# Kernel optimization log

Measured on AMD Instinct MI355X. Metric: run time of the kernel, lower is better.

## Reference

```python
import jax, jax.numpy as jnp
import numpy as np

B, S, IN_DIM, D, H, L, C = 8, 1024, 256, 1024, 16, 6, 10
DK = D // H
EPS = 1e-5


def setup_inputs() -> dict:
    key = jax.random.key(0)
    ks = iter(jax.random.split(key, 64))
    n = lambda shape, s=0.02: jax.random.normal(next(ks), shape, dtype=jnp.float32) * s
    inp = {
        'x': jax.random.normal(next(ks), (B, S, IN_DIM), dtype=jnp.float32),
        'emb_w': n((IN_DIM, D)), 'emb_b': jnp.zeros((D,), jnp.float32),
        'Wq': n((L, D, D)), 'bq': jnp.zeros((L, D), jnp.float32),
        'Wk': n((L, D, D)), 'bk': jnp.zeros((L, D), jnp.float32),
        'Wv': n((L, D, D)), 'bv': jnp.zeros((L, D), jnp.float32),
        'Wo': n((L, D, D)), 'bo': jnp.zeros((L, D), jnp.float32),
        'W1': n((L, D, 4 * D)), 'b1': jnp.zeros((L, 4 * D), jnp.float32),
        'W2': n((L, 4 * D, D)), 'b2': jnp.zeros((L, D), jnp.float32),
        'ln1_s': jnp.ones((L, D), jnp.float32), 'ln1_b': jnp.zeros((L, D), jnp.float32),
        'ln2_s': jnp.ones((L, D), jnp.float32), 'ln2_b': jnp.zeros((L, D), jnp.float32),
        'fc_w': n((D, C)), 'fc_b': jnp.zeros((C,), jnp.float32),
    }
    return inp


def _pos_encoding_rows(n_rows):
    # Faithful to the torch module: pe is [max_len,1,D]; pe[:x.size(0)] picks the
    # first `batch` positions and broadcasts over the sequence dim.
    pos = jnp.arange(n_rows, dtype=jnp.float32)[:, None]
    div = jnp.exp(jnp.arange(0, D, 2, dtype=jnp.float32) * (-np.log(10000.0) / D))
    pe = jnp.zeros((n_rows, D), jnp.float32)
    pe = pe.at[:, 0::2].set(jnp.sin(pos * div)).at[:, 1::2].set(jnp.cos(pos * div))
    return pe


def _layer_norm(x, scale, bias):
    mu = jnp.mean(x, axis=-1, keepdims=True)
    var = jnp.mean(jnp.square(x - mu), axis=-1, keepdims=True)
    return (x - mu) * jax.lax.rsqrt(var + EPS) * scale + bias


def reference(x, emb_w, emb_b, Wq, bq, Wk, bk, Wv, bv, Wo, bo,
              W1, b1, W2, b2, ln1_s, ln1_b, ln2_s, ln2_b, fc_w, fc_b):
    h = x @ emb_w + emb_b                              # [B,S,D]
    h = h + _pos_encoding_rows(B)[:, None, :]          # broadcast pe[:B] over seq
    scale = 1.0 / np.sqrt(DK)
    for i in range(L):
        def heads(y, W, b):
            return (y @ W + b).reshape(B, S, H, DK).transpose(0, 2, 1, 3)  # bhsd
        q = heads(h, Wq[i], bq[i])
        k = heads(h, Wk[i], bk[i])
        v = heads(h, Wv[i], bv[i])
        scores = jnp.einsum('bhqd,bhkd->bhqk', q, k) * scale
        p = jax.nn.softmax(scores, axis=-1)
        o = jnp.einsum('bhqk,bhkd->bhqd', p, v)
        o = o.transpose(0, 2, 1, 3).reshape(B, S, D)
        attn_out = o @ Wo[i] + bo[i]
        h = _layer_norm(h + attn_out, ln1_s[i], ln1_b[i])
        ff = jax.nn.relu(h @ W1[i] + b1[i]) @ W2[i] + b2[i]
        h = _layer_norm(h + ff, ln2_s[i], ln2_b[i])
    pooled = jnp.mean(h, axis=1)                       # [B,D]
    return pooled @ fc_w + fc_b                        # [B,C]
```

## Files before the change

### kernel.cpp

```cpp
#include <hip/hip_runtime.h>
#include <stdint.h>

#define B_   8
#define S_   1024
#define IND  256
#define D_   1024
#define H_   16
#define DKH  64
#define L_   6
#define FF   4096
#define NTOK (B_*S_)

typedef __bf16 bf16;
typedef __attribute__((ext_vector_type(4))) float  f32x4;
typedef __attribute__((ext_vector_type(8))) __bf16 bf16x8;
typedef __attribute__((ext_vector_type(4))) __bf16 bf16x4;
typedef __attribute__((ext_vector_type(2))) __bf16 bf16x2;

#define AS1 __attribute__((address_space(1)))
#define AS3 __attribute__((address_space(3)))

__device__ __forceinline__ void gload16(const void* g, void* l) {
  __builtin_amdgcn_global_load_lds((AS1 void*)(const_cast<void*>(g)), (AS3 void*)l, 16, 0, 0);
}

__global__ __launch_bounds__(256)
void k_trans(const float* __restrict__ in, bf16* __restrict__ out,
             int K, int N, long inStride, long outStride) {
  __shared__ float t[32][33];
  const float* inp = in + (long)blockIdx.z * inStride;
  bf16* outp = out + (long)blockIdx.z * outStride;
  const int n0 = blockIdx.x * 32, k0 = blockIdx.y * 32;
  const int tx = threadIdx.x & 31, ty = threadIdx.x >> 5;
  #pragma unroll
  for (int j = 0; j < 32; j += 8)
    t[ty + j][tx] = inp[(long)(k0 + ty + j) * N + n0 + tx];
  __syncthreads();
  #pragma unroll
  for (int j = 0; j < 32; j += 8)
    outp[(long)(n0 + ty + j) * K + k0 + tx] = (bf16)t[tx][ty + j];
}

__global__ __launch_bounds__(256)
void k_f2b(const float* __restrict__ in, bf16* __restrict__ out) {
  const long i = ((long)blockIdx.x * 256 + threadIdx.x) * 4;
  f32x4 v = *(const f32x4*)(in + i);
  bf16x4 o;
  #pragma unroll
  for (int j = 0; j < 4; ++j) o[j] = (bf16)v[j];
  *(bf16x4*)(out + i) = o;
}

__global__ __launch_bounds__(256)
void k_pe(float* __restrict__ pe) {
  const int i = blockIdx.x * 256 + threadIdx.x;
  const int b = i >> 10, d = i & 1023;
  const float k2 = (float)(d & ~1);
  const float dv = __expf(k2 * (-9.210340371976184f / (float)D_));
  const float a = (float)b * dv;
  pe[i] = (d & 1) ? cosf(a) : sinf(a);
}

__global__ __launch_bounds__(256)
void k_packb(const float* __restrict__ bq, const float* __restrict__ bk,
             const float* __restrict__ bv, float* __restrict__ out) {
  const int i = blockIdx.x * 256 + threadIdx.x;
  const int l = i / 3072, j = i % 3072;
  const float* src = (j < 1024) ? bq : ((j < 2048) ? bk : bv);
  out[i] = src[l * 1024 + (j & 1023)];
}

template<int EPI>
__global__ __launch_bounds__(256)
void k_gemm(const bf16* __restrict__ A, const bf16* __restrict__ Bt,
            const float* __restrict__ bias,
            void* __restrict__ out0, void* __restrict__ out1,
            const float* __restrict__ pe,
            int M, int N, int K) {
  __shared__ __align__(16) bf16 sA[128 * 32];
  __shared__ __align__(16) bf16 sB[128 * 32];
  const int tid = threadIdx.x;
  const int lane = tid & 63, wv = tid >> 6;
  const int bx = blockIdx.x, by = blockIdx.y;
  const int wm = wv >> 1, wn = wv & 1;
  const int lg = lane >> 4, lc = lane & 15;
  const long arow0 = (long)by * 128;
  const long brow0 = (long)bx * 128;
  const int c0 = (wv * 2 + 0) * 64 + lane;
  const int c1 = (wv * 2 + 1) * 64 + lane;
  const int r0 = c0 >> 2, s0 = c0 & 3;
  const int r1 = c1 >> 2, s1 = c1 & 3;
  bf16* ldsA0 = sA + (wv * 2 + 0) * 512;
  bf16* ldsA1 = sA + (wv * 2 + 1) * 512;
  bf16* ldsB0 = sB + (wv * 2 + 0) * 512;
  bf16* ldsB1 = sB + (wv * 2 + 1) * 512;
  const bf16* Ab = A + arow0 * K;
  const bf16* Bb = Bt + brow0 * K;
  f32x4 acc[4][4] = {};
  const int kT = K >> 5;
  for (int kt = 0; kt < kT; ++kt) {
    const int k0 = kt << 5;
    gload16(Ab + (long)r0 * K + k0 + s0 * 8, ldsA0);
    gload16(Ab + (long)r1 * K + k0 + s1 * 8, ldsA1);
    gload16(Bb + (long)r0 * K + k0 + s0 * 8, ldsB0);
    gload16(Bb + (long)r1 * K + k0 + s1 * 8, ldsB1);
    __syncthreads();
    bf16x8 af[4], bfr[4];
    #pragma unroll
    for (int mr = 0; mr < 4; ++mr)
      af[mr] = *(const bf16x8*)(sA + (wm * 64 + mr * 16 + lc) * 32 + lg * 8);
    #pragma unroll
    for (int nc = 0; nc < 4; ++nc)
      bfr[nc] = *(const bf16x8*)(sB + (wn * 64 + nc * 16 + lc) * 32 + lg * 8);
    #pragma unroll
    for (int mr = 0; mr < 4; ++mr)
      #pragma unroll
      for (int nc = 0; nc < 4; ++nc)
        acc[mr][nc] = __builtin_amdgcn_mfma_f32_16x16x32_bf16(af[mr], bfr[nc], acc[mr][nc], 0, 0, 0);
    __syncthreads();
  }
  #pragma unroll
  for (int mr = 0; mr < 4; ++mr) {
    const int row0 = by * 128 + wm * 64 + mr * 16 + lg * 4;
    #pragma unroll
    for (int nc = 0; nc < 4; ++nc) {
      const int col = bx * 128 + wn * 64 + nc * 16 + lc;
      const float bvv = bias[col];
      #pragma unroll
      for (int r = 0; r < 4; ++r) {
        float v = acc[mr][nc][r] + bvv;
        const long rr = row0 + r;
        if constexpr (EPI == 0) {
          ((bf16*)out0)[rr * N + col] = (bf16)v;
        } else {
          const long bb = rr >> 10;
          v += pe[bb * D_ + col];
          ((float*)out0)[rr * N + col] = v;
          ((bf16*)out1)[rr * N + col] = (bf16)v;
        }
      }
    }
  }
}

template<int EPI, int SPLIT>
__global__ __launch_bounds__(512, 2)
void k_gemm256(const bf16* __restrict__ A, const bf16* __restrict__ Bt,
               const float* __restrict__ bias,
               void* __restrict__ out0, void* __restrict__ out1,
               float* __restrict__ pout0, float* __restrict__ pout1,
               int M, int N, int K) {
  __shared__ __align__(16) bf16 lds[65536];
  const int tid = threadIdx.x;
  const int lane = tid & 63, wv = tid >> 6;
  const int wm = wv >> 2, wn = wv & 3;
  const int lg = lane >> 4, lc = lane & 15;
  const int gx = gridDim.x;
  const int nwg = gx * gridDim.y;
  int bid = blockIdx.x + blockIdx.y * gx;
  const int cpx = nwg >> 3;
  bid = (bid & 7) * cpx + (bid >> 3);
  const int bxs = bid % gx, bys = bid / gx;
  const int tileRow = bys * 256, tileCol = bxs * 256;
  const int kHalf = SPLIT ? (K >> 1) : K;
  const long kOff = SPLIT ? (long)blockIdx.z * kHalf : 0;
  const bf16* Abase = A + (long)tileRow * K + kOff;
  const bf16* Bbase = Bt + (long)tileCol * K + kOff;
  const long laneOff = (long)lc * K + lg * 8;
  f32x4 acc[8][4] = {};
  const int NT = kHalf >> 6;
  const int NI = NT >> 1;

  auto stA = [&](int t, int h, int bb) {
    const int rg = h * 16 + wv * 2;
    const int mb = rg >> 1;
    const bf16* s = Abase + (long)(mb * 16) * K + t * 64 + laneOff;
    bf16* d = lds + bb * 32768 + rg * 512;
    gload16(s, d);
    gload16(s + 32, d + 512);
  };
  auto stB = [&](int t, int h, int bb) {
    const int rg = h * 16 + wv * 2;
    const int mb = rg >> 1;
    const bf16* s = Bbase + (long)(mb * 16) * K + t * 64 + laneOff;
    bf16* d = lds + bb * 32768 + 16384 + rg * 512;
    gload16(s, d);
    gload16(s + 32, d + 512);
  };

  bf16x8 aF[8];
  bf16x8 bF0[4], bF1[4];

#define LDA(BB, MH) do { _Pragma("unroll") for (int m = 0; m < 4; ++m) \
    _Pragma("unroll") for (int kk = 0; kk < 2; ++kk) \
      aF[m*2+kk] = *(const bf16x8*)(lds + (BB)*32768 + ((wm*8 + (MH)*4 + m)*2 + kk)*512 + lane*8); \
  } while(0)
#define LDB(BB, NH, DST) do { _Pragma("unroll") for (int n = 0; n < 2; ++n) \
    _Pragma("unroll") for (int kk = 0; kk < 2; ++kk) \
      DST[n*2+kk] = *(const bf16x8*)(lds + (BB)*32768 + 16384 + ((wn*4 + (NH)*2 + n)*2 + kk)*512 + lane*8); \
  } while(0)
#define MMA(MH, NH, BSRC) do { \
    __builtin_amdgcn_s_setprio(1); \
    _Pragma("unroll") for (int m = 0; m < 4; ++m) \
      _Pragma("unroll") for (int n = 0; n < 2; ++n) { \
        acc[(MH)*4+m][(NH)*2+n] = __builtin_amdgcn_mfma_f32_16x16x32_bf16(aF[m*2+0], BSRC[n*2+0], acc[(MH)*4+m][(NH)*2+n], 0, 0, 0); \
        acc[(MH)*4+m][(NH)*2+n] = __builtin_amdgcn_mfma_f32_16x16x32_bf16(aF[m*2+1], BSRC[n*2+1], acc[(MH)*4+m][(NH)*2+n], 0, 0, 0); \
      } \
    __builtin_amdgcn_s_setprio(0); \
  } while(0)
#define VM8 asm volatile("s_waitcnt vmcnt(8)" ::: "memory")
#define VM0 asm volatile("s_waitcnt vmcnt(0)" ::: "memory")
#define BAR __builtin_amdgcn_s_barrier()

  stA(0, 0, 0); stB(0, 0, 0); stA(0, 1, 0); stB(0, 1, 0);
  stA(1, 0, 1); stB(1, 0, 1); stA(1, 1, 1); stB(1, 1, 1);

  for (int i = 0; i < NI - 1; ++i) {
    const int t2 = 2 * i + 2, t3 = 2 * i + 3;
    VM8; BAR; LDA(0, 0); LDB(0, 0, bF0);                    MMA(0, 0, bF0);
         BAR; LDB(0, 1, bF1); stA(t2, 0, 0);                MMA(0, 1, bF1);
         BAR; LDA(0, 1);      stB(t2, 0, 0);                MMA(1, 0, bF0);
         BAR;                 stA(t2, 1, 0); stB(t2, 1, 0); MMA(1, 1, bF1);
    VM8; BAR; LDA(1, 0); LDB(1, 0, bF0);                    MMA(0, 0, bF0);
         BAR; LDB(1, 1, bF1); stA(t3, 0, 1);                MMA(0, 1, bF1);
         BAR; LDA(1, 1);      stB(t3, 0, 1);                MMA(1, 0, bF0);
         BAR;                 stA(t3, 1, 1); stB(t3, 1, 1); MMA(1, 1, bF1);
  }
  {
    VM8; BAR; LDA(0, 0); LDB(0, 0, bF0); MMA(0, 0, bF0);
         BAR; LDB(0, 1, bF1);            MMA(0, 1, bF1);
         BAR; LDA(0, 1);                 MMA(1, 0, bF0);
         BAR;                            MMA(1, 1, bF1);
    VM0; BAR; LDA(1, 0); LDB(1, 0, bF0); MMA(0, 0, bF0);
         BAR; LDB(1, 1, bF1);            MMA(0, 1, bF1);
         BAR; LDA(1, 1);                 MMA(1, 0, bF0);
         BAR;                            MMA(1, 1, bF1);
  }
#undef LDA
#undef LDB
#undef MMA
#undef VM8
#undef VM0
#undef BAR

  #pragma unroll
  for (int mr = 0; mr < 8; ++mr) {
    const int row0 = tileRow + wm * 128 + mr * 16 + lg * 4;
    #pragma unroll
    for (int nr = 0; nr < 4; ++nr) {
      const int col = tileCol + wn * 64 + nr * 16 + lc;
      if constexpr (SPLIT) {
        float* po = blockIdx.z ? pout1 : pout0;
        #pragma unroll
        for (int r = 0; r < 4; ++r)
          po[(long)(row0 + r) * N + col] = acc[mr][nr][r];
      } else if constexpr (EPI == 2) {
        const float bvv = bias[col];
        const int which = col >> 10;
        const int hh = (col & 1023) >> 6;
        const int dk = col & 63;
        const long bb = row0 >> 10;
        const int sr = row0 & 1023;
        if (which == 2) {
          bf16x4 pk;
          #pragma unroll
          for (int r = 0; r < 4; ++r) pk[r] = (bf16)(acc[mr][nr][r] + bvv);
          *(bf16x4*)((bf16*)out1 + ((bb * H_ + hh) * (long)DKH + dk) * S_ + sr) = pk;
        } else {
          #pragma unroll
          for (int r = 0; r < 4; ++r) {
            float v = acc[mr][nr][r] + bvv;
            if (which == 0) v *= 0.125f;
            ((bf16*)out0)[(long)which * NTOK * D_ + ((bb * H_ + hh) * (long)S_ + sr + r) * DKH + dk] = (bf16)v;
          }
        }
      } else {
        const float bvv = bias[col];
        #pragma unroll
        for (int r = 0; r < 4; ++r) {
          float v = acc[mr][nr][r] + bvv;
          const long rr = row0 + r;
          if constexpr (EPI == 1) v = fmaxf(v, 0.f);
          ((bf16*)out0)[rr * N + col] = (bf16)v;
        }
      }
    }
  }
}

__global__ __launch_bounds__(256)
void k_flash(const bf16* __restrict__ qg, const bf16* __restrict__ kgl,
             const bf16* __restrict__ vtg, bf16* __restrict__ og) {
  __shared__ __align__(16) bf16 sK[64 * 64];
  __shared__ __align__(16) bf16 sV[64 * 64];
  __shared__ __align__(16) bf16 sP[4 * 16 * 64];
  const int tid = threadIdx.x, lane = tid & 63, wv = tid >> 6;
  const int lg = lane >> 4, lc = lane & 15;
  int bid = blockIdx.x + blockIdx.y * 16;
  bid = (bid & 7) * 256 + (bid >> 3);
  const int qt = bid & 15, bh = bid >> 4;
  const long base = (long)bh * S_ * DKH;
  const bf16* qb = qg + base;
  const bf16* kb = kgl + base;
  const bf16* vb = vtg + base;
  const int qrow = qt * 64 + wv * 16 + lc;
  const bf16x8 qf0 = *(const bf16x8*)(qb + (long)qrow * DKH + lg * 8);
  const bf16x8 qf1 = *(const bf16x8*)(qb + (long)qrow * DKH + 32 + lg * 8);
  float mrun = -3e38f, lrun = 0.f;
  f32x4 oacc[4] = {};
  bf16* sPw = sP + wv * (16 * 64);
  const int swzP = (lc & 7) << 4;
  const int c0 = wv * 128 + lane, c1 = c0 + 64;
  const int r0 = c0 >> 3, sl0 = (c0 & 7) ^ (r0 & 7);
  const int r1 = c1 >> 3, sl1 = (c1 & 7) ^ (r1 & 7);
  bf16* dst0 = sK + c0 * 8 - lane * 8;
  bf16* dst1 = sK + c1 * 8 - lane * 8;
  bf16* dstV0 = sV + c0 * 8 - lane * 8;
  bf16* dstV1 = sV + c1 * 8 - lane * 8;
  for (int kt = 0; kt < S_ / 64; ++kt) {
    const int gk = kt * 64;
    gload16(kb + (long)(gk + r0) * DKH + sl0 * 8, dst0);
    gload16(kb + (long)(gk + r1) * DKH + sl1 * 8, dst1);
    gload16(vb + (long)r0 * S_ + gk + sl0 * 8, dstV0);
    gload16(vb + (long)r1 * S_ + gk + sl1 * 8, dstV1);
    __syncthreads();
    f32x4 sacc[4] = {};
    #pragma unroll
    for (int nc = 0; nc < 4; ++nc) {
      const int kr = nc * 16 + lc;
      bf16x8 k0 = *(const bf16x8*)((char*)sK + kr * 128 + (((0 + lg) ^ (kr & 7)) << 4));
      bf16x8 k1 = *(const bf16x8*)((char*)sK + kr * 128 + (((4 + lg) ^ (kr & 7)) << 4));
      sacc[nc] = __builtin_amdgcn_mfma_f32_16x16x32_bf16(k0, qf0, sacc[nc], 0, 0, 0);
      sacc[nc] = __builtin_amdgcn_mfma_f32_16x16x32_bf16(k1, qf1, sacc[nc], 0, 0, 0);
    }
    float pm = sacc[0][0];
    #pragma unroll
    for (int nc = 0; nc < 4; ++nc)
      #pragma unroll
      for (int r = 0; r < 4; ++r) pm = fmaxf(pm, sacc[nc][r]);
    pm = fmaxf(pm, __shfl_xor(pm, 16));
    pm = fmaxf(pm, __shfl_xor(pm, 32));
    const float mnew = fmaxf(mrun, pm);
    const float fac = __expf(mrun - mnew);
    float ps = 0.f;
    #pragma unroll
    for (int nc = 0; nc < 4; ++nc)
      #pragma unroll
      for (int r = 0; r < 4; ++r) {
        const float p = __expf(sacc[nc][r] - mnew);
        sacc[nc][r] = p;
        ps += p;
      }
    ps += __shfl_xor(ps, 16);
    ps += __shfl_xor(ps, 32);
    lrun = lrun * fac + ps;
    mrun = mnew;
    #pragma unroll
    for (int nc = 0; nc < 4; ++nc)
      #pragma unroll
      for (int rp = 0; rp < 2; ++rp) {
        bf16x2 t;
        t[0] = (bf16)sacc[nc][rp * 2 + 0];
        t[1] = (bf16)sacc[nc][rp * 2 + 1];
        *(bf16x2*)((char*)sPw + lc * 128 + ((nc * 32 + lg * 8 + rp * 4) ^ swzP)) = t;
      }
    asm volatile("s_waitcnt lgkmcnt(0)" ::: "memory");
    __builtin_amdgcn_sched_barrier(0);
    float fr[4];
    #pragma unroll
    for (int r = 0; r < 4; ++r) fr[r] = __shfl(fac, lg * 4 + r);
    #pragma unroll
    for (int nc = 0; nc < 4; ++nc)
      #pragma unroll
      for (int r = 0; r < 4; ++r) oacc[nc][r] *= fr[r];
    #pragma unroll
    for (int m = 0; m < 2; ++m) {
      const bf16x8 pf = *(const bf16x8*)((char*)sPw + lc * 128 + ((m * 64 + lg * 16) ^ swzP));
      #pragma unroll
      for (int nc = 0; nc < 4; ++nc) {
        const int vr = nc * 16 + lc;
        bf16x8 vf = *(const bf16x8*)((char*)sV + vr * 128 + (((m * 4 + lg) ^ (vr & 7)) << 4));
        oacc[nc] = __builtin_amdgcn_mfma_f32_16x16x32_bf16(pf, vf, oacc[nc], 0, 0, 0);
      }
    }
    __syncthreads();
  }
  const int b = bh >> 4, h = bh & 15;
  const float linv = 1.f / lrun;
  #pragma unroll
  for (int r = 0; r < 4; ++r) {
    const float inv = __shfl(linv, lg * 4 + r);
    const int s = qt * 64 + wv * 16 + lg * 4 + r;
    const long obase = (((long)b * S_ + s) * H_ + h) * DKH;
    #pragma unroll
    for (int nc = 0; nc < 4; ++nc)
      og[obase + nc * 16 + lc] = (bf16)(oacc[nc][r] * inv);
  }
}

template<int TWO>
__global__ __launch_bounds__(256)
void k_addln(const float* __restrict__ hin, const bf16* __restrict__ dlt,
             const float* __restrict__ p0, const float* __restrict__ p1,
             const float* __restrict__ gb,
             const float* __restrict__ sc, const float* __restrict__ bi,
             float* __restrict__ hout, bf16* __restrict__ hbout) {
  const int row = blockIdx.x, t = threadIdx.x;
  const long off = (long)row * D_ + t * 4;
  f32x4 hv = *(const f32x4*)(hin + off);
  f32x4 x;
  if constexpr (TWO) {
    f32x4 a = *(const f32x4*)(p0 + off);
    f32x4 b = *(const f32x4*)(p1 + off);
    f32x4 g = *(const f32x4*)(gb + t * 4);
    #pragma unroll
    for (int j = 0; j < 4; ++j) x[j] = hv[j] + a[j] + b[j] + g[j];
  } else {
    bf16x4 dv = *(const bf16x4*)(dlt + off);
    #pragma unroll
    for (int j = 0; j < 4; ++j) x[j] = hv[j] + (float)dv[j];
  }
  float s = 0.f, ss = 0.f;
  #pragma unroll
  for (int j = 0; j < 4; ++j) { s += x[j]; ss += x[j] * x[j]; }
  #pragma unroll
  for (int m = 1; m < 64; m <<= 1) { s += __shfl_xor(s, m); ss += __shfl_xor(ss, m); }
  __shared__ float red[8];
  const int w = t >> 6, ln = t & 63;
  if (ln == 0) { red[w] = s; red[4 + w] = ss; }
  __syncthreads();
  s = red[0] + red[1] + red[2] + red[3];
  ss = red[4] + red[5] + red[6] + red[7];
  const float mu = s * (1.f / D_);
  const float rstd = rsqrtf(ss * (1.f / D_) - mu * mu + 1e-5f);
  f32x4 scv = *(const f32x4*)(sc + t * 4);
  f32x4 biv = *(const f32x4*)(bi + t * 4);
  f32x4 y; bf16x4 yb;
  #pragma unroll
  for (int j = 0; j < 4; ++j) { y[j] = (x[j] - mu) * rstd * scv[j] + biv[j]; yb[j] = (bf16)y[j]; }
  *(f32x4*)(hout + off) = y;
  *(bf16x4*)(hbout + off) = yb;
}

__global__ __launch_bounds__(256)
void k_pool1(const float* __restrict__ h, float* __restrict__ part) {
  const int i = blockIdx.x * 256 + threadIdx.x;
  const int b = i >> 10, d = i & 1023;
  const int s0 = blockIdx.y * 128;
  float s = 0.f;
  for (int t = 0; t < 128; ++t) s += h[((long)b * S_ + s0 + t) * D_ + d];
  part[(long)blockIdx.y * NTOK + i] = s;
}

__global__ __launch_bounds__(256)
void k_pool2(const float* __restrict__ part, float* __restrict__ pooled) {
  const int i = blockIdx.x * 256 + threadIdx.x;
  float s = 0.f;
  #pragma unroll
  for (int j = 0; j < 8; ++j) s += part[(long)j * NTOK + i];
  pooled[i] = s * (1.f / S_);
}

__global__ __launch_bounds__(64)
void k_fc(const float* __restrict__ pooled, const float* __restrict__ fw,
          const float* __restrict__ fb, float* __restrict__ out) {
  const int b = blockIdx.x / 10, c = blockIdx.x % 10;
  const int lane = threadIdx.x;
  float s = 0.f;
  for (int d = lane; d < D_; d += 64) s += pooled[b * D_ + d] * fw[d * 10 + c];
  #pragma unroll
  for (int m = 1; m < 64; m <<= 1) s += __shfl_xor(s, m);
  if (lane == 0) out[b * 10 + c] = s + fb[c];
}

extern "C" void kernel_launch(void* const* d_in, const int* in_sizes, int n_in,
                              void* d_out, int out_size, void* d_ws, size_t ws_size,
                              hipStream_t stream) {
  const float* x     = (const float*)d_in[0];
  const float* emb_w = (const float*)d_in[1];
  const float* emb_b = (const float*)d_in[2];
  const float* Wq    = (const float*)d_in[3];
  const float* bq    = (const float*)d_in[4];
  const float* Wk    = (const float*)d_in[5];
  const float* bk    = (const float*)d_in[6];
  const float* Wv    = (const float*)d_in[7];
  const float* bv    = (const float*)d_in[8];
  const float* Wo    = (const float*)d_in[9];
  const float* bo    = (const float*)d_in[10];
  const float* W1    = (const float*)d_in[11];
  const float* b1    = (const float*)d_in[12];
  const float* W2    = (const float*)d_in[13];
  const float* b2    = (const float*)d_in[14];
  const float* ln1s  = (const float*)d_in[15];
  const float* ln1b  = (const float*)d_in[16];
  const float* ln2s  = (const float*)d_in[17];
  const float* ln2b  = (const float*)d_in[18];
  const float* fcw   = (const float*)d_in[19];
  const float* fcb   = (const float*)d_in[20];

  char* w = (char*)d_ws;
  size_t off = 0;
  auto alloc = [&](size_t bytes) -> char* {
    char* p = w + off;
    off += (bytes + 255) & ~(size_t)255;
    return p;
  };
  bf16*  x_bf  = (bf16*) alloc((size_t)NTOK * IND * 2);
  bf16*  embT  = (bf16*) alloc((size_t)D_ * IND * 2);
  bf16*  qkvT  = (bf16*) alloc((size_t)L_ * 3 * D_ * D_ * 2);
  bf16*  woT   = (bf16*) alloc((size_t)L_ * D_ * D_ * 2);
  bf16*  w1T   = (bf16*) alloc((size_t)L_ * FF * D_ * 2);
  bf16*  w2T   = (bf16*) alloc((size_t)L_ * D_ * FF * 2);
  float* qkvB  = (float*)alloc((size_t)L_ * 3 * D_ * 4);
  float* pe    = (float*)alloc((size_t)B_ * D_ * 4);
  float* h_f   = (float*)alloc((size_t)NTOK * D_ * 4);
  bf16*  h_b   = (bf16*) alloc((size_t)NTOK * D_ * 2);
  bf16*  delta = (bf16*) alloc((size_t)NTOK * D_ * 2);
  float* pooled= (float*)alloc((size_t)B_ * D_ * 4);
  float* part  = (float*)alloc((size_t)8 * NTOK * 4);
  bf16*  scratch = (bf16*)alloc((size_t)NTOK * FF * 2);
  bf16* qb  = scratch;
  bf16* kb  = scratch + (size_t)NTOK * D_;
  bf16* vTb = scratch + (size_t)2 * NTOK * D_;
  bf16* ob  = scratch + (size_t)3 * NTOK * D_;
  bf16* ffn1 = scratch;
  float* p0 = (float*)alloc((size_t)NTOK * D_ * 4);
  float* p1 = (float*)alloc((size_t)NTOK * D_ * 4);
  const bool canSplit = (off <= ws_size);
  (void)in_sizes; (void)n_in; (void)out_size;

  k_f2b<<<dim3(NTOK * IND / 1024), dim3(256), 0, stream>>>(x, x_bf);
  k_trans<<<dim3(D_ / 32, IND / 32, 1), dim3(256), 0, stream>>>(emb_w, embT, IND, D_, 0, 0);
  k_trans<<<dim3(32, 32, L_), dim3(256), 0, stream>>>(Wq, qkvT,               D_, D_, (long)D_ * D_, (long)3 * D_ * D_);
  k_trans<<<dim3(32, 32, L_), dim3(256), 0, stream>>>(Wk, qkvT + D_ * D_,     D_, D_, (long)D_ * D_, (long)3 * D_ * D_);
  k_trans<<<dim3(32, 32, L_), dim3(256), 0, stream>>>(Wv, qkvT + 2 * D_ * D_, D_, D_, (long)D_ * D_, (long)3 * D_ * D_);
  k_trans<<<dim3(32, 32, L_), dim3(256), 0, stream>>>(Wo, woT, D_, D_, (long)D_ * D_, (long)D_ * D_);
  k_trans<<<dim3(FF / 32, 32, L_), dim3(256), 0, stream>>>(W1, w1T, D_, FF, (long)D_ * FF, (long)FF * D_);
  k_trans<<<dim3(32, FF / 32, L_), dim3(256), 0, stream>>>(W2, w2T, FF, D_, (long)FF * D_, (long)D_ * FF);
  k_pe<<<dim3(B_ * D_ / 256), dim3(256), 0, stream>>>(pe);
  k_packb<<<dim3(L_ * 3 * D_ / 256), dim3(256), 0, stream>>>(bq, bk, bv, qkvB);

  k_gemm<3><<<dim3(D_ / 128, NTOK / 128), dim3(256), 0, stream>>>(
      x_bf, embT, emb_b, h_f, h_b, pe, NTOK, D_, IND);

  for (int l = 0; l < L_; ++l) {
    k_gemm256<2, 0><<<dim3(3 * D_ / 256, NTOK / 256), dim3(512), 0, stream>>>(
        h_b, qkvT + (size_t)l * 3 * D_ * D_, qkvB + l * 3 * D_,
        qb, vTb, nullptr, nullptr, NTOK, 3 * D_, D_);
    k_flash<<<dim3(S_ / 64, B_ * H_), dim3(256), 0, stream>>>(qb, kb, vTb, ob);
    if (canSplit) {
      k_gemm256<0, 1><<<dim3(D_ / 256, NTOK / 256, 2), dim3(512), 0, stream>>>(
          ob, woT + (size_t)l * D_ * D_, nullptr,
          nullptr, nullptr, p0, p1, NTOK, D_, D_);
      k_addln<1><<<dim3(NTOK), dim3(256), 0, stream>>>(
          h_f, nullptr, p0, p1, bo + l * D_, ln1s + l * D_, ln1b + l * D_, h_f, h_b);
    } else {
      k_gemm256<0, 0><<<dim3(D_ / 256, NTOK / 256), dim3(512), 0, stream>>>(
          ob, woT + (size_t)l * D_ * D_, bo + l * D_,
          delta, nullptr, nullptr, nullptr, NTOK, D_, D_);
      k_addln<0><<<dim3(NTOK), dim3(256), 0, stream>>>(
          h_f, delta, nullptr, nullptr, nullptr, ln1s + l * D_, ln1b + l * D_, h_f, h_b);
    }
    k_gemm256<1, 0><<<dim3(FF / 256, NTOK / 256), dim3(512), 0, stream>>>(
        h_b, w1T + (size_t)l * FF * D_, b1 + l * FF,
        ffn1, nullptr, nullptr, nullptr, NTOK, FF, D_);
    if (canSplit) {
      k_gemm256<0, 1><<<dim3(D_ / 256, NTOK / 256, 2), dim3(512), 0, stream>>>(
          ffn1, w2T + (size_t)l * D_ * FF, nullptr,
          nullptr, nullptr, p0, p1, NTOK, D_, FF);
      k_addln<1><<<dim3(NTOK), dim3(256), 0, stream>>>(
          h_f, nullptr, p0, p1, b2 + l * D_, ln2s + l * D_, ln2b + l * D_, h_f, h_b);
    } else {
      k_gemm256<0, 0><<<dim3(D_ / 256, NTOK / 256), dim3(512), 0, stream>>>(
          ffn1, w2T + (size_t)l * D_ * FF, b2 + l * D_,
          delta, nullptr, nullptr, nullptr, NTOK, D_, FF);
      k_addln<0><<<dim3(NTOK), dim3(256), 0, stream>>>(
          h_f, delta, nullptr, nullptr, nullptr, ln2s + l * D_, ln2b + l * D_, h_f, h_b);
    }
  }

  k_pool1<<<dim3(NTOK / 256, 8), dim3(256), 0, stream>>>(h_f, part);
  k_pool2<<<dim3(NTOK / 256), dim3(256), 0, stream>>>(part, pooled);
  k_fc<<<dim3(B_ * 10), dim3(64), 0, stream>>>(pooled, fcw, fcb, (float*)d_out);
}
```

Measured before the change: 2.358 ms.

## Restructure 256x256 GEMM mainloop into 4-slot K=32 ring-buffer pipeline

```diff
diff --git a/kernel.cpp b/kernel.cpp
--- a/kernel.cpp
+++ b/kernel.cpp
@@ -162,86 +162,61 @@
   bid = (bid & 7) * cpx + (bid >> 3);
   const int bxs = bid % gx, bys = bid / gx;
   const int tileRow = bys * 256, tileCol = bxs * 256;
-  const int kHalf = SPLIT ? (K >> 1) : K;
-  const long kOff = SPLIT ? (long)blockIdx.z * kHalf : 0;
+  const int kPart = SPLIT ? (K >> 1) : K;
+  const long kOff = SPLIT ? (long)blockIdx.z * kPart : 0;
   const bf16* Abase = A + (long)tileRow * K + kOff;
   const bf16* Bbase = Bt + (long)tileCol * K + kOff;
   const long laneOff = (long)lc * K + lg * 8;
   f32x4 acc[8][4] = {};
-  const int NT = kHalf >> 6;
-  const int NI = NT >> 1;
-
-  auto stA = [&](int t, int h, int bb) {
-    const int rg = h * 16 + wv * 2;
-    const int mb = rg >> 1;
-    const bf16* s = Abase + (long)(mb * 16) * K + t * 64 + laneOff;
-    bf16* d = lds + bb * 32768 + rg * 512;
-    gload16(s, d);
-    gload16(s + 32, d + 512);
+  const int NT = kPart >> 5;
+
+  const int rgA = wv * 2;
+  auto stage = [&](int t) {
+    const int slot = (t & 3) * 16384;
+    const bf16* sa = Abase + (long)(rgA * 16) * K + t * 32 + laneOff;
+    const bf16* sb = Bbase + (long)(rgA * 16) * K + t * 32 + laneOff;
+    gload16(sa,                lds + slot + rgA * 512);
+    gload16(sa + (long)16 * K, lds + slot + rgA * 512 + 512);
+    gload16(sb,                lds + slot + 8192 + rgA * 512);
+    gload16(sb + (long)16 * K, lds + slot + 8192 + rgA * 512 + 512);
   };
-  auto stB = [&](int t, int h, int bb) {
-    const int rg = h * 16 + wv * 2;
-    const int mb = rg >> 1;
-    const bf16* s = Bbase + (long)(mb * 16) * K + t * 64 + laneOff;
-    bf16* d = lds + bb * 32768 + 16384 + rg * 512;
-    gload16(s, d);
-    gload16(s + 32, d + 512);
+
+  auto compute = [&](int t, bool doStage, int ts) {
+    const int slot = (t & 3) * 16384;
+    __builtin_amdgcn_s_barrier();
+    __builtin_amdgcn_sched_barrier(0);
+    if (doStage) stage(ts);
+    bf16x8 aF[8], bF[4];
+    #pragma unroll
+    for (int m = 0; m < 8; ++m)
+      aF[m] = *(const bf16x8*)(lds + slot + (wm * 8 + m) * 512 + lane * 8);
+    #pragma unroll
+    for (int n = 0; n < 4; ++n)
+      bF[n] = *(const bf16x8*)(lds + slot + 8192 + (wn * 4 + n) * 512 + lane * 8);
+    __builtin_amdgcn_sched_barrier(0);
+    __builtin_amdgcn_s_setprio(1);
+    #pragma unroll
+    for (int m = 0; m < 8; ++m)
+      #pragma unroll
+      for (int n = 0; n < 4; ++n)
+        acc[m][n] = __builtin_amdgcn_mfma_f32_16x16x32_bf16(aF[m], bF[n], acc[m][n], 0, 0, 0);
+    __builtin_amdgcn_s_setprio(0);
   };
 
-  bf16x8 aF[8];
-  bf16x8 bF0[4], bF1[4];
-
-#define LDA(BB, MH) do { _Pragma("unroll") for (int m = 0; m < 4; ++m) \
-    _Pragma("unroll") for (int kk = 0; kk < 2; ++kk) \
-      aF[m*2+kk] = *(const bf16x8*)(lds + (BB)*32768 + ((wm*8 + (MH)*4 + m)*2 + kk)*512 + lane*8); \
-  } while(0)
-#define LDB(BB, NH, DST) do { _Pragma("unroll") for (int n = 0; n < 2; ++n) \
-    _Pragma("unroll") for (int kk = 0; kk < 2; ++kk) \
-      DST[n*2+kk] = *(const bf16x8*)(lds + (BB)*32768 + 16384 + ((wn*4 + (NH)*2 + n)*2 + kk)*512 + lane*8); \
-  } while(0)
-#define MMA(MH, NH, BSRC) do { \
-    __builtin_amdgcn_s_setprio(1); \
-    _Pragma("unroll") for (int m = 0; m < 4; ++m) \
-      _Pragma("unroll") for (int n = 0; n < 2; ++n) { \
-        acc[(MH)*4+m][(NH)*2+n] = __builtin_amdgcn_mfma_f32_16x16x32_bf16(aF[m*2+0], BSRC[n*2+0], acc[(MH)*4+m][(NH)*2+n], 0, 0, 0); \
-        acc[(MH)*4+m][(NH)*2+n] = __builtin_amdgcn_mfma_f32_16x16x32_bf16(aF[m*2+1], BSRC[n*2+1], acc[(MH)*4+m][(NH)*2+n], 0, 0, 0); \
-      } \
-    __builtin_amdgcn_s_setprio(0); \
-  } while(0)
 #define VM8 asm volatile("s_waitcnt vmcnt(8)" ::: "memory")
+#define VM4 asm volatile("s_waitcnt vmcnt(4)" ::: "memory")
 #define VM0 asm volatile("s_waitcnt vmcnt(0)" ::: "memory")
-#define BAR __builtin_amdgcn_s_barrier()
-
-  stA(0, 0, 0); stB(0, 0, 0); stA(0, 1, 0); stB(0, 1, 0);
-  stA(1, 0, 1); stB(1, 0, 1); stA(1, 1, 1); stB(1, 1, 1);
-
-  for (int i = 0; i < NI - 1; ++i) {
-    const int t2 = 2 * i + 2, t3 = 2 * i + 3;
-    VM8; BAR; LDA(0, 0); LDB(0, 0, bF0);                    MMA(0, 0, bF0);
-         BAR; LDB(0, 1, bF1); stA(t2, 0, 0);                MMA(0, 1, bF1);
-         BAR; LDA(0, 1);      stB(t2, 0, 0);                MMA(1, 0, bF0);
-         BAR;                 stA(t2, 1, 0); stB(t2, 1, 0); MMA(1, 1, bF1);
-    VM8; BAR; LDA(1, 0); LDB(1, 0, bF0);                    MMA(0, 0, bF0);
-         BAR; LDB(1, 1, bF1); stA(t3, 0, 1);                MMA(0, 1, bF1);
-         BAR; LDA(1, 1);      stB(t3, 0, 1);                MMA(1, 0, bF0);
-         BAR;                 stA(t3, 1, 1); stB(t3, 1, 1); MMA(1, 1, bF1);
-  }
-  {
-    VM8; BAR; LDA(0, 0); LDB(0, 0, bF0); MMA(0, 0, bF0);
-         BAR; LDB(0, 1, bF1);            MMA(0, 1, bF1);
-         BAR; LDA(0, 1);                 MMA(1, 0, bF0);
-         BAR;                            MMA(1, 1, bF1);
-    VM0; BAR; LDA(1, 0); LDB(1, 0, bF0); MMA(0, 0, bF0);
-         BAR; LDB(1, 1, bF1);            MMA(0, 1, bF1);
-         BAR; LDA(1, 1);                 MMA(1, 0, bF0);
-         BAR;                            MMA(1, 1, bF1);
-  }
-#undef LDA
-#undef LDB
-#undef MMA
+
+  stage(0); stage(1); stage(2);
+  int t = 0;
+  for (; t < NT - 3; ++t) { VM8; compute(t, true, t + 3); }
+  VM8; compute(NT - 3, false, 0);
+  VM4; compute(NT - 2, false, 0);
+  VM0; compute(NT - 1, false, 0);
+
 #undef VM8
+#undef VM4
 #undef VM0
-#undef BAR
 
   #pragma unroll
   for (int mr = 0; mr < 8; ++mr) {
```

After: 2.392 ms. Within noise of the previous version (+1.5%).

## Restructure GEMM main loop into explicit barrier-bracketed phases with full-tile staging

Applied to the files above, without the earlier changes.

```diff
diff --git a/kernel.cpp b/kernel.cpp
--- a/kernel.cpp
+++ b/kernel.cpp
@@ -162,30 +162,27 @@
   bid = (bid & 7) * cpx + (bid >> 3);
   const int bxs = bid % gx, bys = bid / gx;
   const int tileRow = bys * 256, tileCol = bxs * 256;
-  const int kHalf = SPLIT ? (K >> 1) : K;
-  const long kOff = SPLIT ? (long)blockIdx.z * kHalf : 0;
+  const int kPart = SPLIT ? (K >> 1) : K;
+  const long kOff = SPLIT ? (long)blockIdx.z * kPart : 0;
   const bf16* Abase = A + (long)tileRow * K + kOff;
   const bf16* Bbase = Bt + (long)tileCol * K + kOff;
   const long laneOff = (long)lc * K + lg * 8;
   f32x4 acc[8][4] = {};
-  const int NT = kHalf >> 6;
+  const int NT = kPart >> 6;
   const int NI = NT >> 1;
 
-  auto stA = [&](int t, int h, int bb) {
-    const int rg = h * 16 + wv * 2;
-    const int mb = rg >> 1;
-    const bf16* s = Abase + (long)(mb * 16) * K + t * 64 + laneOff;
-    bf16* d = lds + bb * 32768 + rg * 512;
-    gload16(s, d);
-    gload16(s + 32, d + 512);
-  };
-  auto stB = [&](int t, int h, int bb) {
-    const int rg = h * 16 + wv * 2;
-    const int mb = rg >> 1;
-    const bf16* s = Bbase + (long)(mb * 16) * K + t * 64 + laneOff;
-    bf16* d = lds + bb * 32768 + 16384 + rg * 512;
-    gload16(s, d);
-    gload16(s + 32, d + 512);
+  auto stageFull = [&](int t, int bb) {
+    #pragma unroll
+    for (int h = 0; h < 2; ++h) {
+      const int rg = h * 16 + wv * 2;
+      const int mb = rg >> 1;
+      const bf16* sa = Abase + (long)(mb * 16) * K + t * 64 + laneOff;
+      const bf16* sb = Bbase + (long)(mb * 16) * K + t * 64 + laneOff;
+      bf16* da = lds + bb * 32768 + rg * 512;
+      bf16* db = lds + bb * 32768 + 16384 + rg * 512;
+      gload16(sa, da);      gload16(sa + 32, da + 512);
+      gload16(sb, db);      gload16(sb + 32, db + 512);
+    }
   };
 
   bf16x8 aF[8];
@@ -200,48 +197,69 @@
       DST[n*2+kk] = *(const bf16x8*)(lds + (BB)*32768 + 16384 + ((wn*4 + (NH)*2 + n)*2 + kk)*512 + lane*8); \
   } while(0)
 #define MMA(MH, NH, BSRC) do { \
-    __builtin_amdgcn_s_setprio(1); \
     _Pragma("unroll") for (int m = 0; m < 4; ++m) \
       _Pragma("unroll") for (int n = 0; n < 2; ++n) { \
         acc[(MH)*4+m][(NH)*2+n] = __builtin_amdgcn_mfma_f32_16x16x32_bf16(aF[m*2+0], BSRC[n*2+0], acc[(MH)*4+m][(NH)*2+n], 0, 0, 0); \
         acc[(MH)*4+m][(NH)*2+n] = __builtin_amdgcn_mfma_f32_16x16x32_bf16(aF[m*2+1], BSRC[n*2+1], acc[(MH)*4+m][(NH)*2+n], 0, 0, 0); \
       } \
+  } while(0)
+#define PH_R(RD, MH, NH, BSRC) do { \
+    RD; \
+    __builtin_amdgcn_sched_barrier(0); \
+    __builtin_amdgcn_s_barrier(); \
+    asm volatile("s_waitcnt lgkmcnt(0)" ::: "memory"); \
+    __builtin_amdgcn_sched_barrier(0); \
+    __builtin_amdgcn_s_setprio(1); \
+    MMA(MH, NH, BSRC); \
     __builtin_amdgcn_s_setprio(0); \
+    __builtin_amdgcn_s_barrier(); \
   } while(0)
-#define VM8 asm volatile("s_waitcnt vmcnt(8)" ::: "memory")
-#define VM0 asm volatile("s_waitcnt vmcnt(0)" ::: "memory")
-#define BAR __builtin_amdgcn_s_barrier()
-
-  stA(0, 0, 0); stB(0, 0, 0); stA(0, 1, 0); stB(0, 1, 0);
-  stA(1, 0, 1); stB(1, 0, 1); stA(1, 1, 1); stB(1, 1, 1);
+#define PH_S(STG, VMW, MH, NH, BSRC) do { \
+    STG; \
+    asm volatile("s_waitcnt " VMW ::: "memory"); \
+    __builtin_amdgcn_sched_barrier(0); \
+    __builtin_amdgcn_s_barrier(); \
+    __builtin_amdgcn_s_setprio(1); \
+    MMA(MH, NH, BSRC); \
+    __builtin_amdgcn_s_setprio(0); \
+    __builtin_amdgcn_s_barrier(); \
+  } while(0)
+
+  stageFull(0, 0);
+  stageFull(1, 1);
+  asm volatile("s_waitcnt vmcnt(8)" ::: "memory");
+  __builtin_amdgcn_s_barrier();
 
   for (int i = 0; i < NI - 1; ++i) {
     const int t2 = 2 * i + 2, t3 = 2 * i + 3;
-    VM8; BAR; LDA(0, 0); LDB(0, 0, bF0);                    MMA(0, 0, bF0);
-         BAR; LDB(0, 1, bF1); stA(t2, 0, 0);                MMA(0, 1, bF1);
-         BAR; LDA(0, 1);      stB(t2, 0, 0);                MMA(1, 0, bF0);
-         BAR;                 stA(t2, 1, 0); stB(t2, 1, 0); MMA(1, 1, bF1);
-    VM8; BAR; LDA(1, 0); LDB(1, 0, bF0);                    MMA(0, 0, bF0);
-         BAR; LDB(1, 1, bF1); stA(t3, 0, 1);                MMA(0, 1, bF1);
-         BAR; LDA(1, 1);      stB(t3, 0, 1);                MMA(1, 0, bF0);
-         BAR;                 stA(t3, 1, 1); stB(t3, 1, 1); MMA(1, 1, bF1);
+    PH_R(LDA(0, 0); LDB(0, 0, bF0), 0, 0, bF0);
+    PH_R(LDB(0, 1, bF1),            0, 1, bF1);
+    PH_R(LDA(0, 1),                 1, 0, bF0);
+    PH_S(stageFull(t2, 0), "vmcnt(8)", 1, 1, bF1);
+    PH_R(LDA(1, 0); LDB(1, 0, bF0), 0, 0, bF0);
+    PH_R(LDB(1, 1, bF1),            0, 1, bF1);
+    PH_R(LDA(1, 1),                 1, 0, bF0);
+    PH_S(stageFull(t3, 1), "vmcnt(8)", 1, 1, bF1);
   }
   {
-    VM8; BAR; LDA(0, 0); LDB(0, 0, bF0); MMA(0, 0, bF0);
-         BAR; LDB(0, 1, bF1);            MMA(0, 1, bF1);
-         BAR; LDA(0, 1);                 MMA(1, 0, bF0);
-         BAR;                            MMA(1, 1, bF1);
-    VM0; BAR; LDA(1, 0); LDB(1, 0, bF0); MMA(0, 0, bF0);
-         BAR; LDB(1, 1, bF1);            MMA(0, 1, bF1);
-         BAR; LDA(1, 1);                 MMA(1, 0, bF0);
-         BAR;                            MMA(1, 1, bF1);
+    PH_R(LDA(0, 0); LDB(0, 0, bF0), 0, 0, bF0);
+    PH_R(LDB(0, 1, bF1),            0, 1, bF1);
+    PH_R(LDA(0, 1),                 1, 0, bF0);
+    PH_S(, "vmcnt(0)", 1, 1, bF1);
+    PH_R(LDA(1, 0); LDB(1, 0, bF0), 0, 0, bF0);
+    PH_R(LDB(1, 1, bF1),            0, 1, bF1);
+    PH_R(LDA(1, 1),                 1, 0, bF0);
+    {
+      __builtin_amdgcn_s_setprio(1);
+      MMA(1, 1, bF1);
+      __builtin_amdgcn_s_setprio(0);
+    }
   }
 #undef LDA
 #undef LDB
 #undef MMA
-#undef VM8
-#undef VM0
-#undef BAR
+#undef PH_R
+#undef PH_S
 
   #pragma unroll
   for (int mr = 0; mr < 8; ++mr) {
```

Measured after the change: 2.612 ms. 10.8% more time.

## Double-buffer flash attention K/V tiles and batch GEMM stage loads

Applied to the files above, without the earlier changes.

```diff
diff --git a/kernel.cpp b/kernel.cpp
--- a/kernel.cpp
+++ b/kernel.cpp
@@ -162,30 +162,27 @@
   bid = (bid & 7) * cpx + (bid >> 3);
   const int bxs = bid % gx, bys = bid / gx;
   const int tileRow = bys * 256, tileCol = bxs * 256;
-  const int kHalf = SPLIT ? (K >> 1) : K;
-  const long kOff = SPLIT ? (long)blockIdx.z * kHalf : 0;
+  const int kPart = SPLIT ? (K >> 1) : K;
+  const long kOff = SPLIT ? (long)blockIdx.z * kPart : 0;
   const bf16* Abase = A + (long)tileRow * K + kOff;
   const bf16* Bbase = Bt + (long)tileCol * K + kOff;
   const long laneOff = (long)lc * K + lg * 8;
   f32x4 acc[8][4] = {};
-  const int NT = kHalf >> 6;
+  const int NT = kPart >> 6;
   const int NI = NT >> 1;
 
-  auto stA = [&](int t, int h, int bb) {
-    const int rg = h * 16 + wv * 2;
-    const int mb = rg >> 1;
-    const bf16* s = Abase + (long)(mb * 16) * K + t * 64 + laneOff;
-    bf16* d = lds + bb * 32768 + rg * 512;
-    gload16(s, d);
-    gload16(s + 32, d + 512);
-  };
-  auto stB = [&](int t, int h, int bb) {
-    const int rg = h * 16 + wv * 2;
-    const int mb = rg >> 1;
-    const bf16* s = Bbase + (long)(mb * 16) * K + t * 64 + laneOff;
-    bf16* d = lds + bb * 32768 + 16384 + rg * 512;
-    gload16(s, d);
-    gload16(s + 32, d + 512);
+  auto stageFull = [&](int t, int bb) {
+    #pragma unroll
+    for (int h = 0; h < 2; ++h) {
+      const int rg = h * 16 + wv * 2;
+      const int mb = rg >> 1;
+      const bf16* sa = Abase + (long)(mb * 16) * K + t * 64 + laneOff;
+      const bf16* sb = Bbase + (long)(mb * 16) * K + t * 64 + laneOff;
+      bf16* da = lds + bb * 32768 + rg * 512;
+      bf16* db = lds + bb * 32768 + 16384 + rg * 512;
+      gload16(sa, da);      gload16(sa + 32, da + 512);
+      gload16(sb, db);      gload16(sb + 32, db + 512);
+    }
   };
 
   bf16x8 aF[8];
@@ -212,19 +209,19 @@
 #define VM0 asm volatile("s_waitcnt vmcnt(0)" ::: "memory")
 #define BAR __builtin_amdgcn_s_barrier()
 
-  stA(0, 0, 0); stB(0, 0, 0); stA(0, 1, 0); stB(0, 1, 0);
-  stA(1, 0, 1); stB(1, 0, 1); stA(1, 1, 1); stB(1, 1, 1);
+  stageFull(0, 0);
+  stageFull(1, 1);
 
   for (int i = 0; i < NI - 1; ++i) {
     const int t2 = 2 * i + 2, t3 = 2 * i + 3;
-    VM8; BAR; LDA(0, 0); LDB(0, 0, bF0);                    MMA(0, 0, bF0);
-         BAR; LDB(0, 1, bF1); stA(t2, 0, 0);                MMA(0, 1, bF1);
-         BAR; LDA(0, 1);      stB(t2, 0, 0);                MMA(1, 0, bF0);
-         BAR;                 stA(t2, 1, 0); stB(t2, 1, 0); MMA(1, 1, bF1);
-    VM8; BAR; LDA(1, 0); LDB(1, 0, bF0);                    MMA(0, 0, bF0);
-         BAR; LDB(1, 1, bF1); stA(t3, 0, 1);                MMA(0, 1, bF1);
-         BAR; LDA(1, 1);      stB(t3, 0, 1);                MMA(1, 0, bF0);
-         BAR;                 stA(t3, 1, 1); stB(t3, 1, 1); MMA(1, 1, bF1);
+    VM8; BAR; LDA(0, 0); LDB(0, 0, bF0);   MMA(0, 0, bF0);
+         BAR; LDB(0, 1, bF1);              MMA(0, 1, bF1);
+         BAR; LDA(0, 1);                   MMA(1, 0, bF0);
+         BAR; stageFull(t2, 0);            MMA(1, 1, bF1);
+    VM8; BAR; LDA(1, 0); LDB(1, 0, bF0);   MMA(0, 0, bF0);
+         BAR; LDB(1, 1, bF1);              MMA(0, 1, bF1);
+         BAR; LDA(1, 1);                   MMA(1, 0, bF0);
+         BAR; stageFull(t3, 1);            MMA(1, 1, bF1);
   }
   {
     VM8; BAR; LDA(0, 0); LDB(0, 0, bF0); MMA(0, 0, bF0);
@@ -291,8 +288,8 @@
 __global__ __launch_bounds__(256)
 void k_flash(const bf16* __restrict__ qg, const bf16* __restrict__ kgl,
              const bf16* __restrict__ vtg, bf16* __restrict__ og) {
-  __shared__ __align__(16) bf16 sK[64 * 64];
-  __shared__ __align__(16) bf16 sV[64 * 64];
+  __shared__ __align__(16) bf16 sK[2][64 * 64];
+  __shared__ __align__(16) bf16 sV[2][64 * 64];
   __shared__ __align__(16) bf16 sP[4 * 16 * 64];
   const int tid = threadIdx.x, lane = tid & 63, wv = tid >> 6;
   const int lg = lane >> 4, lc = lane & 15;
@@ -313,23 +310,33 @@
   const int c0 = wv * 128 + lane, c1 = c0 + 64;
   const int r0 = c0 >> 3, sl0 = (c0 & 7) ^ (r0 & 7);
   const int r1 = c1 >> 3, sl1 = (c1 & 7) ^ (r1 & 7);
-  bf16* dst0 = sK + c0 * 8 - lane * 8;
-  bf16* dst1 = sK + c1 * 8 - lane * 8;
-  bf16* dstV0 = sV + c0 * 8 - lane * 8;
-  bf16* dstV1 = sV + c1 * 8 - lane * 8;
+  const int dOff0 = c0 * 8 - lane * 8;
+  const int dOff1 = c1 * 8 - lane * 8;
+  auto stage = [&](int kt, int b) {
+    const int gk = kt * 64;
+    gload16(kb + (long)(gk + r0) * DKH + sl0 * 8, &sK[b][dOff0]);
+    gload16(kb + (long)(gk + r1) * DKH + sl1 * 8, &sK[b][dOff1]);
+    gload16(vb + (long)r0 * S_ + gk + sl0 * 8, &sV[b][dOff0]);
+    gload16(vb + (long)r1 * S_ + gk + sl1 * 8, &sV[b][dOff1]);
+  };
+  stage(0, 0);
   for (int kt = 0; kt < S_ / 64; ++kt) {
-    const int gk = kt * 64;
-    gload16(kb + (long)(gk + r0) * DKH + sl0 * 8, dst0);
-    gload16(kb + (long)(gk + r1) * DKH + sl1 * 8, dst1);
-    gload16(vb + (long)r0 * S_ + gk + sl0 * 8, dstV0);
-    gload16(vb + (long)r1 * S_ + gk + sl1 * 8, dstV1);
-    __syncthreads();
+    const int cur = kt & 1;
+    if (kt + 1 < S_ / 64) {
+      stage(kt + 1, cur ^ 1);
+      asm volatile("s_waitcnt vmcnt(4)" ::: "memory");
+    } else {
+      asm volatile("s_waitcnt vmcnt(0)" ::: "memory");
+    }
+    __builtin_amdgcn_s_barrier();
+    const bf16* sKc = sK[cur];
+    const bf16* sVc = sV[cur];
     f32x4 sacc[4] = {};
     #pragma unroll
     for (int nc = 0; nc < 4; ++nc) {
       const int kr = nc * 16 + lc;
-      bf16x8 k0 = *(const bf16x8*)((char*)sK + kr * 128 + (((0 + lg) ^ (kr & 7)) << 4));
-      bf16x8 k1 = *(const bf16x8*)((char*)sK + kr * 128 + (((4 + lg) ^ (kr & 7)) << 4));
+      bf16x8 k0 = *(const bf16x8*)((char*)sKc + kr * 128 + (((0 + lg) ^ (kr & 7)) << 4));
+      bf16x8 k1 = *(const bf16x8*)((char*)sKc + kr * 128 + (((4 + lg) ^ (kr & 7)) << 4));
       sacc[nc] = __builtin_amdgcn_mfma_f32_16x16x32_bf16(k0, qf0, sacc[nc], 0, 0, 0);
       sacc[nc] = __builtin_amdgcn_mfma_f32_16x16x32_bf16(k1, qf1, sacc[nc], 0, 0, 0);
     }
@@ -379,11 +386,11 @@
       #pragma unroll
       for (int nc = 0; nc < 4; ++nc) {
         const int vr = nc * 16 + lc;
-        bf16x8 vf = *(const bf16x8*)((char*)sV + vr * 128 + (((m * 4 + lg) ^ (vr & 7)) << 4));
+        bf16x8 vf = *(const bf16x8*)((char*)sVc + vr * 128 + (((m * 4 + lg) ^ (vr & 7)) << 4));
         oacc[nc] = __builtin_amdgcn_mfma_f32_16x16x32_bf16(pf, vf, oacc[nc], 0, 0, 0);
       }
     }
-    __syncthreads();
+    __builtin_amdgcn_s_barrier();
   }
   const int b = bh >> 4, h = bh & 15;
   const float linv = 1.f / lrun;
```

New measurement: 2.505 ms. 1.06x slower.
